# Optimization experiments

Hardware: AMD Instinct MI355X
Metric: run time of the kernel (lower is better)

Reference implementation:

```python
import jax, jax.numpy as jnp
import numpy as np

B, C, H, W = 4, 16, 320, 640


def _propagate_front(x, g):
    """Linear propagation along leading axis.
    x, g: [L, ...]. out[0] = x[0]; out[i] = x[i]*(1-g[i]) + g[i]*out[i-1].
    """
    def step(prev, xg):
        xr, gr = xg
        out = xr * (1.0 - gr) + gr * prev
        return out, out
    _, ys = jax.lax.scan(step, x[0], (x[1:], g[1:]))
    return jnp.concatenate([x[:1], ys], axis=0)


def _propagate(x, g, axis, reverse):
    xm = jnp.moveaxis(x, axis, 0)
    gm = jnp.moveaxis(g, axis, 0)
    if reverse:
        xm = xm[::-1]
        gm = gm[::-1]
    ym = _propagate_front(xm, gm)
    if reverse:
        ym = ym[::-1]
    return jnp.moveaxis(ym, 0, axis)


def setup_inputs() -> dict:
    key = jax.random.key(0)
    ks = jax.random.split(key, 5)
    shape = (B, C, H, W)
    return {
        "input": jax.random.normal(ks[0], shape, dtype=jnp.float32),
        "g0": jax.random.uniform(ks[1], shape, dtype=jnp.float32),
        "g1": jax.random.uniform(ks[2], shape, dtype=jnp.float32),
        "g2": jax.random.uniform(ks[3], shape, dtype=jnp.float32),
        "g3": jax.random.uniform(ks[4], shape, dtype=jnp.float32),
    }


def reference(input, g0, g1, g2, g3):
    # 4-directional gated recurrent grid propagation, fused by elementwise max.
    r_down = _propagate(input, g0, axis=2, reverse=False)   # top -> bottom over H
    r_up = _propagate(input, g1, axis=2, reverse=True)      # bottom -> top over H
    r_right = _propagate(input, g2, axis=3, reverse=False)  # left -> right over W
    r_left = _propagate(input, g3, axis=3, reverse=True)    # right -> left over W
    return jnp.maximum(jnp.maximum(jnp.maximum(r_down, r_up), r_right), r_left)
```

## Files before the change

kernel.cpp:

```cpp
#include <hip/hip_runtime.h>

constexpr int Bn = 4;
constexpr int Cn = 16;
constexpr int Hn = 320;
constexpr int Wn = 640;
constexpr int NCOL = Bn * Cn * Wn;
constexpr int NROW = Bn * Cn * Hn;

constexpr int HS = 20;
constexpr int NS = 16;
constexpr int GPW = Wn / 64;

__global__ __launch_bounds__(1024, 8) void vert_both(
    const float* __restrict__ x, const float* __restrict__ g0,
    const float* __restrict__ g1, float* __restrict__ vm) {
  __shared__ float As[NS][64], Bs[NS][64];
  const int grp = blockIdx.x;
  const int bc = grp / GPW;
  const int w0 = (grp % GPW) * 64;
  const int s = threadIdx.x >> 6;
  const int l = threadIdx.x & 63;
  const int colbase = bc * (Hn * Wn) + w0 + l;

  float y[HS], P[HS];

  {
    int off = colbase + (s * HS) * Wn;
    float yy = 0.0f, pp = 1.0f;
#pragma unroll
    for (int i = 0; i < HS; ++i) {
      float xv = x[off];
      float gv = g0[off];
      float bb = (s == 0 && i == 0) ? 0.0f : gv;
      yy = fmaf(bb, yy - xv, xv);
      pp *= bb;
      y[i] = yy;
      P[i] = pp;
      off += Wn;
    }
    As[s][l] = yy;
    Bs[s][l] = pp;
  }
  __syncthreads();
  if (threadIdx.x < 64) {
    float c = 0.0f;
#pragma unroll
    for (int ss = 0; ss < NS; ++ss) {
      float a = As[ss][l], b = Bs[ss][l];
      As[ss][l] = c;
      c = fmaf(b, c, a);
    }
  }
  __syncthreads();
  {
    float c = As[s][l];
    int off = colbase + (s * HS) * Wn;
#pragma unroll
    for (int i = 0; i < HS; ++i) {
      vm[off] = fmaf(P[i], c, y[i]);
      off += Wn;
    }
  }
  __syncthreads();

  {
    int off = colbase + (Hn - 1 - s * HS) * Wn;
    float yy = 0.0f, pp = 1.0f;
#pragma unroll
    for (int i = 0; i < HS; ++i) {
      float xv = x[off];
      float gv = g1[off];
      float bb = (s == 0 && i == 0) ? 0.0f : gv;
      yy = fmaf(bb, yy - xv, xv);
      pp *= bb;
      y[i] = yy;
      P[i] = pp;
      off -= Wn;
    }
    As[s][l] = yy;
    Bs[s][l] = pp;
  }
  __syncthreads();
  if (threadIdx.x < 64) {
    float c = 0.0f;
#pragma unroll
    for (int ss = 0; ss < NS; ++ss) {
      float a = As[ss][l], b = Bs[ss][l];
      As[ss][l] = c;
      c = fmaf(b, c, a);
    }
  }
  __syncthreads();
  {
    float c = As[s][l];
    int off = colbase + (Hn - 1 - s * HS) * Wn;
#pragma unroll
    for (int i = 0; i < HS; ++i) {
      float u = fmaf(P[i], c, y[i]);
      vm[off] = fmaxf(vm[off], u);
      off -= Wn;
    }
  }
}

constexpr int WSEG = 10;

__global__ __launch_bounds__(256) void horiz_final(
    const float* __restrict__ x, const float* __restrict__ g2,
    const float* __restrict__ g3, const float* __restrict__ vm,
    float* __restrict__ out) {
  __shared__ float xs[4 * Wn], rrs[4 * Wn], rls[4 * Wn];
  const int tid = threadIdx.x, wv = tid >> 6, l = tid & 63;
  const size_t rowbase = (size_t)blockIdx.x * 4 * Wn;

  const float4* xg = (const float4*)(x + rowbase);
  const float4* g2g = (const float4*)(g2 + rowbase);
  const float4* g3g = (const float4*)(g3 + rowbase);
  const float4* vm4 = (const float4*)(vm + rowbase);
  float4* xsv = (float4*)xs;
  float4* rrv = (float4*)rrs;
  float4* rlv = (float4*)rls;

  const int i0 = tid, i1 = tid + 256, i2 = tid + 512;
  float4 v0, v1, v2;
  xsv[i0] = xg[i0]; rrv[i0] = g2g[i0]; rlv[i0] = g3g[i0]; v0 = vm4[i0];
  xsv[i1] = xg[i1]; rrv[i1] = g2g[i1]; rlv[i1] = g3g[i1]; v1 = vm4[i1];
  if (i2 < Wn) { xsv[i2] = xg[i2]; rrv[i2] = g2g[i2]; rlv[i2] = g3g[i2]; v2 = vm4[i2]; }
  __syncthreads();

  const int rb = wv * Wn + l * WSEG;
  float xl[WSEG], gl[WSEG], yl[WSEG], pl[WSEG];
#pragma unroll
  for (int i = 0; i < WSEG; ++i) { xl[i] = xs[rb + i]; gl[i] = rrs[rb + i]; }

  {
    float y = 0.0f, p = 1.0f;
#pragma unroll
    for (int i = 0; i < WSEG; ++i) {
      float bb = (l == 0 && i == 0) ? 0.0f : gl[i];
      y = fmaf(bb, y - xl[i], xl[i]);
      p *= bb;
      yl[i] = y; pl[i] = p;
    }
    float A = y, B = p;
#pragma unroll
    for (int off = 1; off < 64; off <<= 1) {
      float Au = __shfl_up(A, off);
      float Bu = __shfl_up(B, off);
      if (l >= off) { A = fmaf(B, Au, A); B *= Bu; }
    }
    float c = __shfl_up(A, 1);
    if (l == 0) c = 0.0f;
#pragma unroll
    for (int i = 0; i < WSEG; ++i) rrs[rb + i] = fmaf(pl[i], c, yl[i]);
  }

#pragma unroll
  for (int i = 0; i < WSEG; ++i) gl[i] = rls[rb + i];
  {
    float y = 0.0f, p = 1.0f;
#pragma unroll
    for (int i = WSEG - 1; i >= 0; --i) {
      float bb = (l == 63 && i == WSEG - 1) ? 0.0f : gl[i];
      y = fmaf(bb, y - xl[i], xl[i]);
      p *= bb;
      yl[i] = y; pl[i] = p;
    }
    float A = y, B = p;
#pragma unroll
    for (int off = 1; off < 64; off <<= 1) {
      float Ad = __shfl_down(A, off);
      float Bd = __shfl_down(B, off);
      if (l + off < 64) { A = fmaf(B, Ad, A); B *= Bd; }
    }
    float c = __shfl_down(A, 1);
    if (l == 63) c = 0.0f;
#pragma unroll
    for (int i = 0; i < WSEG; ++i) rls[rb + i] = fmaf(pl[i], c, yl[i]);
  }
  __syncthreads();

  float4* o4 = (float4*)(out + rowbase);
  {
    float4 a = rrv[i0], b = rlv[i0];
    float4 o;
    o.x = fmaxf(fmaxf(a.x, b.x), v0.x);
    o.y = fmaxf(fmaxf(a.y, b.y), v0.y);
    o.z = fmaxf(fmaxf(a.z, b.z), v0.z);
    o.w = fmaxf(fmaxf(a.w, b.w), v0.w);
    o4[i0] = o;
  }
  {
    float4 a = rrv[i1], b = rlv[i1];
    float4 o;
    o.x = fmaxf(fmaxf(a.x, b.x), v1.x);
    o.y = fmaxf(fmaxf(a.y, b.y), v1.y);
    o.z = fmaxf(fmaxf(a.z, b.z), v1.z);
    o.w = fmaxf(fmaxf(a.w, b.w), v1.w);
    o4[i1] = o;
  }
  if (i2 < Wn) {
    float4 a = rrv[i2], b = rlv[i2];
    float4 o;
    o.x = fmaxf(fmaxf(a.x, b.x), v2.x);
    o.y = fmaxf(fmaxf(a.y, b.y), v2.y);
    o.z = fmaxf(fmaxf(a.z, b.z), v2.z);
    o.w = fmaxf(fmaxf(a.w, b.w), v2.w);
    o4[i2] = o;
  }
}

extern "C" void kernel_launch(void* const* d_in, const int* in_sizes, int n_in,
                              void* d_out, int out_size, void* d_ws,
                              size_t ws_size, hipStream_t stream) {
  const float* x = (const float*)d_in[0];
  const float* g0 = (const float*)d_in[1];
  const float* g1 = (const float*)d_in[2];
  const float* g2 = (const float*)d_in[3];
  const float* g3 = (const float*)d_in[4];
  float* out = (float*)d_out;

  vert_both<<<NCOL / 64, 1024, 0, stream>>>(x, g0, g1, out);
  horiz_final<<<NROW / 4, 256, 0, stream>>>(x, g2, g3, out, out);
}
```

Before: 277.8 us.

## Keep down-pass results and x in registers to avoid vm round-trip

The vertical kernel now gives each thread the same segment for both the downward and the upward pass. It keeps x and the downward results in registers, so x is loaded once and the intermediate vm write and read-back are gone. The upward pass reverses its segment order in the scan so the thread mapping stays the same. This adds register arrays, so the launch bound is relaxed to 4 blocks per CU to avoid spills, which may lower occupancy.

```diff
diff --git a/kernel.cpp b/kernel.cpp
--- a/kernel.cpp
+++ b/kernel.cpp
@@ -11,7 +11,7 @@
 constexpr int NS = 16;
 constexpr int GPW = Wn / 64;
 
-__global__ __launch_bounds__(1024, 8) void vert_both(
+__global__ __launch_bounds__(1024, 4) void vert_both(
     const float* __restrict__ x, const float* __restrict__ g0,
     const float* __restrict__ g1, float* __restrict__ vm) {
   __shared__ float As[NS][64], Bs[NS][64];
@@ -21,21 +21,25 @@
   const int s = threadIdx.x >> 6;
   const int l = threadIdx.x & 63;
   const int colbase = bc * (Hn * Wn) + w0 + l;
-
-  float y[HS], P[HS];
-
-  {
-    int off = colbase + (s * HS) * Wn;
+  const int base = colbase + (s * HS) * Wn;
+
+  float xl[HS];
+  float rd[HS];
+  float yu[HS];
+  float Pu[HS];
+
+  {
+    int off = base;
     float yy = 0.0f, pp = 1.0f;
 #pragma unroll
     for (int i = 0; i < HS; ++i) {
-      float xv = x[off];
+      xl[i] = x[off];
       float gv = g0[off];
       float bb = (s == 0 && i == 0) ? 0.0f : gv;
-      yy = fmaf(bb, yy - xv, xv);
+      yy = fmaf(bb, yy - xl[i], xl[i]);
       pp *= bb;
-      y[i] = yy;
-      P[i] = pp;
+      rd[i] = yy;
+      yu[i] = pp;
       off += Wn;
     }
     As[s][l] = yy;
@@ -54,27 +58,21 @@
   __syncthreads();
   {
     float c = As[s][l];
-    int off = colbase + (s * HS) * Wn;
-#pragma unroll
-    for (int i = 0; i < HS; ++i) {
-      vm[off] = fmaf(P[i], c, y[i]);
-      off += Wn;
-    }
-  }
-  __syncthreads();
-
-  {
-    int off = colbase + (Hn - 1 - s * HS) * Wn;
+#pragma unroll
+    for (int i = 0; i < HS; ++i) rd[i] = fmaf(yu[i], c, rd[i]);
+  }
+
+  {
+    int off = base + (HS - 1) * Wn;
     float yy = 0.0f, pp = 1.0f;
 #pragma unroll
-    for (int i = 0; i < HS; ++i) {
-      float xv = x[off];
+    for (int i = HS - 1; i >= 0; --i) {
       float gv = g1[off];
-      float bb = (s == 0 && i == 0) ? 0.0f : gv;
-      yy = fmaf(bb, yy - xv, xv);
+      float bb = (s == NS - 1 && i == HS - 1) ? 0.0f : gv;
+      yy = fmaf(bb, yy - xl[i], xl[i]);
       pp *= bb;
-      y[i] = yy;
-      P[i] = pp;
+      yu[i] = yy;
+      Pu[i] = pp;
       off -= Wn;
     }
     As[s][l] = yy;
@@ -84,7 +82,7 @@
   if (threadIdx.x < 64) {
     float c = 0.0f;
 #pragma unroll
-    for (int ss = 0; ss < NS; ++ss) {
+    for (int ss = NS - 1; ss >= 0; --ss) {
       float a = As[ss][l], b = Bs[ss][l];
       As[ss][l] = c;
       c = fmaf(b, c, a);
@@ -93,12 +91,12 @@
   __syncthreads();
   {
     float c = As[s][l];
-    int off = colbase + (Hn - 1 - s * HS) * Wn;
+    int off = base;
 #pragma unroll
     for (int i = 0; i < HS; ++i) {
-      float u = fmaf(P[i], c, y[i]);
-      vm[off] = fmaxf(vm[off], u);
-      off -= Wn;
+      float u = fmaf(Pu[i], c, yu[i]);
+      vm[off] = fmaxf(rd[i], u);
+      off += Wn;
     }
   }
 }
```

Measured after the change: 261.9 us. 1.06x faster.
